# Kernel optimization log

Hardware: AMD Instinct MI355X
Metric: run time of the kernel (lower is better)

The kernel has to match this reference:

```python
import jax, jax.numpy as jnp
import numpy as np

N = 30000   # fluid particles
E = 480000  # edges
F = 4       # fluidFeatures (in channels)
P = 8       # RBF basis size per dim (dims=[8], 1D)
LAYERS = [32, 64, 64, 2]


def hat_basis(x, n):
    # 'linear' RBF: hat functions on n evenly spaced centers in [-1, 1]
    centers = jnp.linspace(-1.0, 1.0, n, dtype=x.dtype)
    spacing = 2.0 / (n - 1)
    return jnp.maximum(0.0, 1.0 - jnp.abs(x[:, None] - centers[None, :]) / spacing)  # [E, n]


def rbf_conv(x, fi, fj, d, W, b, mask, n_nodes):
    # x: [N, Cin]; d: [E, 1] clamped; W: [P, Cin, Cout]; b: [Cout]
    phi = hat_basis(d[:, 0], W.shape[0])      # [E, P]
    xj = x[fj]                                 # gather source features [E, Cin]
    msg = jnp.zeros((xj.shape[0], W.shape[2]), dtype=x.dtype)
    for p in range(W.shape[0]):                # small fixed P=8 loop keeps memory O(E*Cout)
        msg = msg + phi[:, p, None] * (xj @ W[p])
    msg = jnp.where(mask[:, None], msg, 0.0)   # centerIgnore: drop self edges fi==fj
    out = jax.ops.segment_sum(msg, fi, num_segments=n_nodes)  # scatter-reduce to targets
    return out + b


def _xavier(key, shape_in, shape_out):
    lim = float(np.sqrt(6.0 / (shape_in + shape_out)))
    return jax.random.uniform(key, (shape_in, shape_out), jnp.float32, -lim, lim)


def setup_inputs() -> dict:
    key = jax.random.key(0)
    ks = jax.random.split(key, 16)
    fluidFeatures = jax.random.normal(ks[0], (N, F), jnp.float32)
    fi = jax.random.randint(ks[1], (E,), 0, N)
    fj = jax.random.randint(ks[2], (E,), 0, N)
    distances = jax.random.normal(ks[3], (E, 1), jnp.float32)
    # conv channels: 4->32, 64->64, 64->64, 64->2
    cio = [(F, 32), (2 * 32, 64), (64, 64), (64, 2)]
    inp = {"fluidFeatures": fluidFeatures, "fi": fi, "fj": fj, "distances": distances}
    for li, (ci, co) in enumerate(cio):
        inp[f"cW{li}"] = jax.random.normal(ks[4 + li], (P, ci, co), jnp.float32) * (1.0 / np.sqrt(P * ci))
        inp[f"cb{li}"] = jnp.zeros((co,), jnp.float32)
        inp[f"fW{li}"] = _xavier(ks[8 + li], ci, co)   # stored [in, out]
        inp[f"fb{li}"] = jnp.zeros((co,), jnp.float32)
    return inp


def reference(fluidFeatures, fi, fj, distances,
              cW0, cb0, fW0, fb0, cW1, cb1, fW1, fb1,
              cW2, cb2, fW2, fb2, cW3, cb3, fW3, fb3):
    n_nodes = fluidFeatures.shape[0]
    mask = fi != fj                     # centerIgnore (mask instead of filter: jit-safe)
    d = jnp.clip(distances, -1.0, 1.0)

    conv0 = rbf_conv(fluidFeatures, fi, fj, d, cW0, cb0, mask, n_nodes)  # [N, 32]
    lin0 = fluidFeatures @ fW0 + fb0                                      # [N, 32]
    ans = jnp.concatenate([lin0, conv0], axis=1)                          # [N, 64]

    # i = 1: features[0]=32 != features[1]=64 -> no residual
    ansc = jax.nn.relu(ans)
    ans = rbf_conv(ansc, fi, fj, d, cW1, cb1, mask, n_nodes) + (ansc @ fW1 + fb1)
    # i = 2: features[1]==features[2]==64 and shapes match -> residual
    ansc = jax.nn.relu(ans)
    ans = rbf_conv(ansc, fi, fj, d, cW2, cb2, mask, n_nodes) + (ansc @ fW2 + fb2) + ans
    # i = 3: 64 -> 2, no residual
    ansc = jax.nn.relu(ans)
    ans = rbf_conv(ansc, fi, fj, d, cW3, cb3, mask, n_nodes) + (ansc @ fW3 + fb3)

    return ans  # dim == 1 (dims=[8]) -> no /128
```

## Files before the change

kernel.cpp:

```cpp
#include <hip/hip_runtime.h>


#define CAP 48

typedef __attribute__((ext_vector_type(8))) short short8;
typedef __attribute__((ext_vector_type(4))) short short4v;
typedef __attribute__((ext_vector_type(4))) float f32x4;
typedef int v4i __attribute__((ext_vector_type(4)));

__device__ __forceinline__ short bf16s(float f) {
  unsigned u = __float_as_uint(f);
  return (short)((u + 0x7FFF + ((u >> 16) & 1)) >> 16);
}
__device__ __forceinline__ float b2f(unsigned short s) {
  return __uint_as_float(((unsigned)s) << 16);
}
__device__ __forceinline__ unsigned pack2(float a, float b) {
  return (unsigned)(unsigned short)bf16s(a) | ((unsigned)(unsigned short)bf16s(b) << 16);
}
__device__ __forceinline__ float dec_w0(int v) {
  return __uint_as_float(0x3F800000u | (((unsigned)v & 0xFFFu) << 11)) - 1.0f;
}
__device__ __forceinline__ float dec_sf(int v) {
  return (float)(((unsigned)v >> 12) & 1u);
}
__device__ __forceinline__ unsigned long long rfl64(unsigned long long x) {
  unsigned lo = __builtin_amdgcn_readfirstlane((unsigned)x);
  unsigned hi = __builtin_amdgcn_readfirstlane((unsigned)(x >> 32));
  return ((unsigned long long)hi << 32) | (unsigned long long)lo;
}
__device__ __forceinline__ void gload_lds4(const void* g, void* l) {
  __builtin_amdgcn_global_load_lds(
      (const __attribute__((address_space(1))) void*)g,
      (__attribute__((address_space(3))) void*)l, 4, 0, 0);
}

#define WAIT_VM0 asm volatile("s_waitcnt vmcnt(0)" ::: "memory")
#define WAIT_LGKM0 asm volatile("s_waitcnt lgkmcnt(0)" ::: "memory")

#define LOAD_RECS32Q(JROW, CPTR, MRAW)                                      \
  v4i q0, q1, q2, q3, q4, q5, q6, q7;                                       \
  int MRAW;                                                                 \
  asm volatile("s_load_dwordx4 %0, %9, 0x0\n\t"                             \
               "s_load_dwordx4 %1, %9, 0x10\n\t"                            \
               "s_load_dwordx4 %2, %9, 0x20\n\t"                            \
               "s_load_dwordx4 %3, %9, 0x30\n\t"                            \
               "s_load_dwordx4 %4, %9, 0x40\n\t"                            \
               "s_load_dwordx4 %5, %9, 0x50\n\t"                            \
               "s_load_dwordx4 %6, %9, 0x60\n\t"                            \
               "s_load_dwordx4 %7, %9, 0x70\n\t"                            \
               "s_load_dword %8, %10, 0x0\n\t"                              \
               "s_waitcnt lgkmcnt(0)"                                       \
               : "=&s"(q0), "=&s"(q1), "=&s"(q2), "=&s"(q3), "=&s"(q4),     \
                 "=&s"(q5), "=&s"(q6), "=&s"(q7), "=&s"(MRAW)               \
               : "s"(JROW), "s"(CPTR)                                       \
               : "memory")

#define LOAD_RECS16TQ(JROW)                                                 \
  v4i qt0, qt1, qt2, qt3;                                                   \
  asm volatile("s_load_dwordx4 %0, %4, 0x80\n\t"                            \
               "s_load_dwordx4 %1, %4, 0x90\n\t"                            \
               "s_load_dwordx4 %2, %4, 0xA0\n\t"                            \
               "s_load_dwordx4 %3, %4, 0xB0\n\t"                            \
               "s_waitcnt lgkmcnt(0)"                                       \
               : "=&s"(qt0), "=&s"(qt1), "=&s"(qt2), "=&s"(qt3)             \
               : "s"(JROW)                                                  \
               : "memory")

#define RECK(K) ((K) < 4 ? q0[(K) & 3] : (K) < 8 ? q1[(K) & 3] :            \
                 (K) < 12 ? q2[(K) & 3] : (K) < 16 ? q3[(K) & 3] :          \
                 (K) < 20 ? q4[(K) & 3] : (K) < 24 ? q5[(K) & 3] :          \
                 (K) < 28 ? q6[(K) & 3] : q7[(K) & 3])
#define RECT(K) ((K) < 4 ? qt0[(K) & 3] : (K) < 8 ? qt1[(K) & 3] :          \
                 (K) < 12 ? qt2[(K) & 3] : qt3[(K) & 3])

__global__ void fill_prep(const float* __restrict__ dist,
                          const int* __restrict__ fi, const int* __restrict__ fj,
                          int* __restrict__ cnt, int* __restrict__ jw, int nE,
                          const float* __restrict__ cW1, const float* __restrict__ fW1,
                          const float* __restrict__ cW2, const float* __restrict__ fW2,
                          short* __restrict__ wt1, short* __restrict__ wt2,
                          const float* __restrict__ X,
                          const float* __restrict__ cW0,
                          const float* __restrict__ fW0,
                          unsigned short* __restrict__ U0, int n,
                          int fillBlocks, int prepBlocks) {
  if ((int)blockIdx.x < fillBlocks) {
    int e = blockIdx.x * blockDim.x + threadIdx.x;
    if (e >= nE) return;
    int i = fi[e], j = fj[e];
    if (i == j) return;
    float d = fminf(1.0f, fmaxf(-1.0f, dist[e]));
    float u = (d + 1.0f) * 3.5f;
    int p = min((int)u, 6);
    float w0 = 1.0f - (u - (float)p);
    int wq = min((int)(w0 * 4096.0f + 0.5f), 4095);
    unsigned off = (unsigned)(j * 9 + p);
    int pos = atomicAdd(&cnt[i], 1);
    if (pos < CAP)
      jw[(size_t)i * CAP + pos] = (int)((off << 13) | 0x1000u | (unsigned)wq);
  } else if ((int)blockIdx.x < fillBlocks + prepBlocks) {
    int idx = ((int)blockIdx.x - fillBlocks) * blockDim.x + threadIdx.x;
    if (idx >= 2 * 576 * 64) return;
    int sel = idx / (576 * 64);
    int r = idx - sel * (576 * 64);
    int col = r >> 6, ch = r & 63;
    const float* cW = sel ? cW2 : cW1;
    const float* fW = sel ? fW2 : fW1;
    float v;
    if (col < 512) {
      int p = col >> 6, co = col & 63;
      v = cW[((size_t)p * 64 + ch) * 64 + co];
    } else {
      v = fW[(size_t)ch * 64 + (col - 512)];
    }
    (sel ? wt2 : wt1)[(size_t)col * 64 + ch] = bf16s(v);
  } else {
    int idx = ((int)blockIdx.x - fillBlocks - prepBlocks) * blockDim.x + threadIdx.x;
    if (idx >= n * 72) return;
    int i = idx / 72, g = idx - i * 72;
    float4 x = *(const float4*)(X + (size_t)i * 4);
    float xk[4] = {x.x, x.y, x.z, x.w};
    float s[4] = {0, 0, 0, 0};
    if (g < 64) {
      int p = g >> 3;
      int co = (g * 4) & 31;
      #pragma unroll
      for (int k = 0; k < 4; ++k) {
        const float* wr = cW0 + ((size_t)p * 4 + k) * 32 + co;
        #pragma unroll
        for (int c = 0; c < 4; ++c) s[c] = fmaf(xk[k], wr[c], s[c]);
      }
    } else {
      int co = (g - 64) * 4;
      #pragma unroll
      for (int k = 0; k < 4; ++k) {
        const float* wr = fW0 + (size_t)k * 32 + co;
        #pragma unroll
        for (int c = 0; c < 4; ++c) s[c] = fmaf(xk[k], wr[c], s[c]);
      }
    }
    uint2 pk = make_uint2(pack2(s[0], s[1]), pack2(s[2], s[3]));
    *(uint2*)(U0 + (size_t)i * 288 + g * 4) = pk;
  }
}

__device__ __forceinline__ void gemm_tail8(const unsigned short* sXa, short* sUL,
                                           const short* __restrict__ WT,
                                           int w, int lane) {
  const int mrow = lane & 15;
  const int quad = lane >> 4;
  short8 b0 = *(const short8*)(sXa + mrow * 64 + quad * 8);
  short8 b1 = *(const short8*)(sXa + mrow * 64 + quad * 8 + 32);
  for (int t = w; t < 36; t += 8) {
    const short* A = WT + (size_t)(t * 16 + mrow) * 64 + quad * 8;
    short8 a0 = *(const short8*)(A);
    short8 a1 = *(const short8*)(A + 32);
    f32x4 acc = {0, 0, 0, 0};
    acc = __builtin_amdgcn_mfma_f32_16x16x32_bf16(a0, b0, acc, 0, 0, 0);
    acc = __builtin_amdgcn_mfma_f32_16x16x32_bf16(a1, b1, acc, 0, 0, 0);
    short4v pk;
    #pragma unroll
    for (int r = 0; r < 4; ++r) pk[r] = bf16s(acc[r]);
    *(short4v*)(sUL + mrow * 584 + t * 16 + quad * 4) = pk;
  }
}

__global__ __launch_bounds__(512, 8) void layer0_gemm(
    const unsigned short* __restrict__ U0,
    const int* __restrict__ cnt, const int* __restrict__ jw,
    const float* __restrict__ cb0, const float* __restrict__ fb0,
    const short* __restrict__ WTul,
    unsigned short* __restrict__ UL, int n) {
  __shared__ __align__(16) char smem[8 * 4096];
  __shared__ __align__(16) unsigned short sXa[16 * 64];
  const int tid = threadIdx.x;
  const int w = tid >> 6;
  const int lane = tid & 63;
  const int grp = lane >> 5;
  const int gl = lane & 31;
  const unsigned gl4 = (unsigned)gl * 4u;
  const int nodeBase = blockIdx.x * 8;
  const int i = nodeBase + w;
  const bool valid = (i < n);
  const int ic = valid ? i : 0;
  if (tid < 256) ((unsigned*)sXa)[256 + tid] = 0u;
  const int* jrow = (const int*)rfl64((unsigned long long)(jw + (size_t)ic * CAP));
  const int* cptr = (const int*)rfl64((unsigned long long)(cnt + ic));
  LOAD_RECS32Q(jrow, cptr, mraw);
  const int m = valid ? min(mraw, CAP) : 0;
  char* ldsW = smem + w * 4096;
  unsigned* ldsWu = (unsigned*)ldsW;
  const char* u0B = (const char*)U0;
  float accLo = 0.0f, accHi = 0.0f;
#define L0_ISSUE(K, RE)                                                     \
  { int v_ = grp ? RE(2 * (K) + 1) : RE(2 * (K));                           \
    unsigned soff_ = (((unsigned)v_) >> 7) & 0xFFFFFFC0u;                   \
    gload_lds4(u0B + soff_ + gl4, ldsW + (K) * 256); }
#define L0_CONS(K, RE)                                                      \
  { int v_ = grp ? RE(2 * (K) + 1) : RE(2 * (K));                           \
    float w0_ = dec_w0(v_);                                                 \
    float wgt_ = (gl < 16) ? w0_ : (dec_sf(v_) - w0_);                      \
    unsigned rd_ = ldsWu[(K) * 64 + lane];                                  \
    accLo = fmaf(wgt_, __uint_as_float(rd_ << 16), accLo);                  \
    accHi = fmaf(wgt_, __uint_as_float(rd_ & 0xFFFF0000u), accHi); }
  if (m > 0) {
    if (m <= 16) {
      #pragma unroll
      for (int k = 0; k < 8; ++k) L0_ISSUE(k, RECK);
      WAIT_VM0;
      #pragma unroll
      for (int k = 0; k < 8; ++k) L0_CONS(k, RECK);
    } else {
      #pragma unroll
      for (int k = 0; k < 16; ++k) L0_ISSUE(k, RECK);
      WAIT_VM0;
      #pragma unroll
      for (int k = 0; k < 16; ++k) L0_CONS(k, RECK);
      if (m > 32) {
        LOAD_RECS16TQ(jrow);
        WAIT_LGKM0;
        #pragma unroll
        for (int k = 0; k < 8; ++k) L0_ISSUE(k, RECT);
        WAIT_VM0;
        #pragma unroll
        for (int k = 0; k < 8; ++k) L0_CONS(k, RECT);
      }
    }
  }
#undef L0_ISSUE
#undef L0_CONS
  accLo += __shfl_xor(accLo, 16, 64);
  accHi += __shfl_xor(accHi, 16, 64);
  accLo += __shfl_xor(accLo, 32, 64);
  accHi += __shfl_xor(accHi, 32, 64);
  if (lane < 16) {
    const int l = lane;
    float c0v = fmaxf(accLo + cb0[2 * l], 0.0f);
    float c1v = fmaxf(accHi + cb0[2 * l + 1], 0.0f);
    unsigned lr = ((const unsigned*)(U0 + (size_t)ic * 288 + 256))[l];
    float l0 = fmaxf(__uint_as_float(lr << 16) + fb0[2 * l], 0.0f);
    float l1 = fmaxf(__uint_as_float(lr & 0xFFFF0000u) + fb0[2 * l + 1], 0.0f);
    unsigned* row = (unsigned*)(sXa + w * 64);
    row[l] = pack2(l0, l1);
    row[16 + l] = pack2(c0v, c1v);
  }
  __syncthreads();

  gemm_tail8(sXa, (short*)smem, WTul, w, lane);
  __syncthreads();
  const int r2 = tid >> 6;
  const int c0 = tid & 63;
  if (nodeBase + r2 < n) {
    const short* sUL = (const short*)smem;
    unsigned short* dst = UL + (size_t)(nodeBase + r2) * 576;
    #pragma unroll
    for (int chunk = c0; chunk < 72; chunk += 64)
      *(short8*)(dst + chunk * 8) = *(const short8*)(sUL + r2 * 584 + chunk * 8);
  }
}

__global__ __launch_bounds__(512, 8) void conv_gemm(
    const unsigned short* __restrict__ ULA,
    const int* __restrict__ cnt, const int* __restrict__ jw,
    const float* __restrict__ cb, const float* __restrict__ fb,
    const short* __restrict__ WTul2,
    float* __restrict__ outAns,
    unsigned short* __restrict__ ULB, int n) {
  __shared__ __align__(16) char smem[8 * 4096];
  __shared__ __align__(16) unsigned short sXa[16 * 64];
  const int tid = threadIdx.x;
  const int w = tid >> 6;
  const int lane = tid & 63;
  const int half = lane >> 5;
  const int pl = lane & 31;
  const unsigned lane4 = (unsigned)lane * 4u;
  const int nodeBase = blockIdx.x * 8;
  const int i = nodeBase + w;
  const bool valid = (i < n);
  const int ic = valid ? i : 0;
  if (tid < 256) ((unsigned*)sXa)[256 + tid] = 0u;
  const int* jrow = (const int*)rfl64((unsigned long long)(jw + (size_t)ic * CAP));
  const int* cptr = (const int*)rfl64((unsigned long long)(cnt + ic));
  LOAD_RECS32Q(jrow, cptr, mraw);
  const int m = valid ? min(mraw, CAP) : 0;
  const unsigned Lraw = ((const unsigned*)(ULA + (size_t)ic * 576 + 512))[pl];
  char* ldsW = smem + w * 4096;
  unsigned* ldsWu = (unsigned*)ldsW;
  const char* ulB = (const char*)ULA;
  float accLo = 0.0f, accHi = 0.0f;
#define CV_ISSUE(K, RE)                                                     \
  { unsigned soff_ = (((unsigned)RE(K)) >> 6) & 0xFFFFFF80u;                \
    gload_lds4(ulB + soff_ + lane4, ldsW + ((K) & 15) * 256); }
#define CV_CONS(K, RE)                                                      \
  { int v_ = RE(K);                                                         \
    float w0_ = dec_w0(v_);                                                 \
    float wv_ = half ? (dec_sf(v_) - w0_) : w0_;                            \
    unsigned rd_ = ldsWu[((K) & 15) * 64 + lane];                           \
    accLo = fmaf(wv_, __uint_as_float(rd_ << 16), accLo);                   \
    accHi = fmaf(wv_, __uint_as_float(rd_ & 0xFFFF0000u), accHi); }
  if (m > 0) {
    #pragma unroll
    for (int k = 0; k < 16; ++k) CV_ISSUE(k, RECK);
    WAIT_VM0;
    #pragma unroll
    for (int k = 0; k < 16; ++k) CV_CONS(k, RECK);
    if (m > 16) {
      WAIT_LGKM0;
      #pragma unroll
      for (int k = 16; k < 32; ++k) CV_ISSUE(k, RECK);
      WAIT_VM0;
      #pragma unroll
      for (int k = 16; k < 32; ++k) CV_CONS(k, RECK);
      if (m > 32) {
        LOAD_RECS16TQ(jrow);
        WAIT_LGKM0;
        #pragma unroll
        for (int k = 0; k < 16; ++k) CV_ISSUE(k, RECT);
        WAIT_VM0;
        #pragma unroll
        for (int k = 0; k < 16; ++k) CV_CONS(k, RECT);
      }
    }
  }
#undef CV_ISSUE
#undef CV_CONS
  accLo += __shfl_xor(accLo, 32, 64);
  accHi += __shfl_xor(accHi, 32, 64);
  if (half == 0) {
    unsigned* row = (unsigned*)(sXa + w * 64);
    if (valid) {
      const int c0i = 2 * pl, c1i = c0i + 1;
      float o0 = accLo + __uint_as_float(Lraw << 16) + cb[c0i] + fb[c0i];
      float o1 = accHi + __uint_as_float(Lraw & 0xFFFF0000u) + cb[c1i] + fb[c1i];
      *(float2*)(outAns + (size_t)i * 64 + c0i) = make_float2(o0, o1);
      row[pl] = pack2(fmaxf(o0, 0.0f), fmaxf(o1, 0.0f));
    } else {
      row[pl] = 0u;
    }
  }
  __syncthreads();

  gemm_tail8(sXa, (short*)smem, WTul2, w, lane);
  __syncthreads();
  const int r2 = tid >> 6;
  const int c0 = tid & 63;
  if (nodeBase + r2 < n) {
    const short* sUL = (const short*)smem;
    unsigned short* dst = ULB + (size_t)(nodeBase + r2) * 576;
    #pragma unroll
    for (int chunk = c0; chunk < 72; chunk += 64)
      *(short8*)(dst + chunk * 8) = *(const short8*)(sUL + r2 * 584 + chunk * 8);
  }
}

__global__ __launch_bounds__(256, 8) void conv2_kernel(
    const unsigned short* __restrict__ UL,
    const int* __restrict__ cnt, const int* __restrict__ jw,
    const float* __restrict__ cb, const float* __restrict__ fb,
    const float* __restrict__ resid,
    const float* __restrict__ cW3,
    float* __restrict__ T,
    unsigned short* __restrict__ outAnsc, int n) {
  __shared__ __align__(16) char smem2[4 * 4096];
  const int lane = threadIdx.x & 63;
  const int half = lane >> 5;
  const int pl = lane & 31;
  const unsigned lane4 = (unsigned)lane * 4u;
  const int w4 = threadIdx.x >> 6;
  const int i = (blockIdx.x * blockDim.x + threadIdx.x) >> 6;
  if (i >= n) return;
  const int* jrow = (const int*)rfl64((unsigned long long)(jw + (size_t)i * CAP));
  const int* cptr = (const int*)rfl64((unsigned long long)(cnt + i));
  LOAD_RECS32Q(jrow, cptr, mraw);
  const int m = min(mraw, CAP);
  const unsigned Lraw = ((const unsigned*)(UL + (size_t)i * 576 + 512))[pl];
  float2 rv = *(const float2*)(resid + (size_t)i * 64 + 2 * pl);
  char* ldsW = smem2 + w4 * 4096;
  unsigned* ldsWu = (unsigned*)ldsW;
  const char* ulB = (const char*)UL;
  float accLo = 0.0f, accHi = 0.0f;
#define CV_ISSUE(K, RE)                                                     \
  { unsigned soff_ = (((unsigned)RE(K)) >> 6) & 0xFFFFFF80u;                \
    gload_lds4(ulB + soff_ + lane4, ldsW + ((K) & 15) * 256); }
#define CV_CONS(K, RE)                                                      \
  { int v_ = RE(K);                                                         \
    float w0_ = dec_w0(v_);                                                 \
    float wv_ = half ? (dec_sf(v_) - w0_) : w0_;                            \
    unsigned rd_ = ldsWu[((K) & 15) * 64 + lane];                           \
    accLo = fmaf(wv_, __uint_as_float(rd_ << 16), accLo);                   \
    accHi = fmaf(wv_, __uint_as_float(rd_ & 0xFFFF0000u), accHi); }
  if (m > 0) {
    #pragma unroll
    for (int k = 0; k < 16; ++k) CV_ISSUE(k, RECK);
    WAIT_VM0;
    #pragma unroll
    for (int k = 0; k < 16; ++k) CV_CONS(k, RECK);
    if (m > 16) {
      WAIT_LGKM0;
      #pragma unroll
      for (int k = 16; k < 32; ++k) CV_ISSUE(k, RECK);
      WAIT_VM0;
      #pragma unroll
      for (int k = 16; k < 32; ++k) CV_CONS(k, RECK);
      if (m > 32) {
        LOAD_RECS16TQ(jrow);
        WAIT_LGKM0;
        #pragma unroll
        for (int k = 0; k < 16; ++k) CV_ISSUE(k, RECT);
        WAIT_VM0;
        #pragma unroll
        for (int k = 0; k < 16; ++k) CV_CONS(k, RECT);
      }
    }
  }
#undef CV_ISSUE
#undef CV_CONS
  accLo += __shfl_xor(accLo, 32, 64);
  accHi += __shfl_xor(accHi, 32, 64);
  if (half == 0) {
    const int c0i = 2 * pl, c1i = c0i + 1;
    float o0 = accLo + __uint_as_float(Lraw << 16) + cb[c0i] + fb[c0i] + rv.x;
    float o1 = accHi + __uint_as_float(Lraw & 0xFFFF0000u) + cb[c1i] + fb[c1i] + rv.y;
    unsigned short xb0 = (unsigned short)bf16s(fmaxf(o0, 0.0f));
    unsigned short xb1 = (unsigned short)bf16s(fmaxf(o1, 0.0f));
    ((unsigned*)(outAnsc + (size_t)i * 64))[pl] = (unsigned)xb0 | ((unsigned)xb1 << 16);
    float x0 = b2f(xb0), x1 = b2f(xb1);
    float c[16];
    #pragma unroll
    for (int t = 0; t < 16; ++t) {
      const float* wrow = cW3 + ((size_t)(t >> 1) * 64) * 2 + (t & 1);
      c[t] = x0 * wrow[c0i * 2] + x1 * wrow[c1i * 2];
    }
    #pragma unroll
    for (int off = 16; off > 0; off >>= 1) {
      #pragma unroll
      for (int t = 0; t < 16; ++t) c[t] += __shfl_xor(c[t], off, 64);
    }
    if (pl == 0) {
      float* tr = T + (size_t)i * 18;
      #pragma unroll
      for (int t = 0; t < 16; ++t) tr[t] = c[t];
    }
  }
}

__global__ __launch_bounds__(256, 4) void layer3_kernel(
    const unsigned short* __restrict__ Xb,
    const float* __restrict__ T,
    const int* __restrict__ cnt, const int* __restrict__ jw,
    const float* __restrict__ cb3, const float* __restrict__ fb3,
    const float* __restrict__ fW3,
    float* __restrict__ out, int n) {
  const int lane = threadIdx.x & 63;
  const int i = (blockIdx.x * blockDim.x + threadIdx.x) >> 6;
  if (i >= n) return;
  const int m = min(cnt[i], CAP);
  float c0 = 0.0f, c1 = 0.0f;
  if (lane < m) {
    int v = jw[(size_t)i * CAP + lane];
    unsigned off = (unsigned)v >> 13;
    float w0 = dec_w0(v);
    float w1 = 1.0f - w0;
    const float* tb = T + (size_t)off * 2;
    float2 ta = *(const float2*)(tb);
    float2 tc = *(const float2*)(tb + 2);
    c0 = w0 * ta.x + w1 * tc.x;
    c1 = w0 * ta.y + w1 * tc.y;
  }
  float xi = b2f(Xb[(size_t)i * 64 + lane]);
  float2 fw = *(const float2*)(fW3 + lane * 2);
  c0 = fmaf(xi, fw.x, c0);
  c1 = fmaf(xi, fw.y, c1);
  #pragma unroll
  for (int off = 32; off > 0; off >>= 1) {
    c0 += __shfl_xor(c0, off, 64);
    c1 += __shfl_xor(c1, off, 64);
  }
  if (lane == 0) {
    out[(size_t)i * 2 + 0] = c0 + cb3[0] + fb3[0];
    out[(size_t)i * 2 + 1] = c1 + cb3[1] + fb3[1];
  }
}

extern "C" void kernel_launch(void* const* d_in, const int* in_sizes, int n_in,
                              void* d_out, int out_size, void* d_ws, size_t ws_size,
                              hipStream_t stream) {
  const float* X    = (const float*)d_in[0];
  const int*   fi   = (const int*)d_in[1];
  const int*   fj   = (const int*)d_in[2];
  const float* dist = (const float*)d_in[3];
  const float* cW0 = (const float*)d_in[4];  const float* cb0 = (const float*)d_in[5];
  const float* fW0 = (const float*)d_in[6];  const float* fb0 = (const float*)d_in[7];
  const float* cW1 = (const float*)d_in[8];  const float* cb1 = (const float*)d_in[9];
  const float* fW1 = (const float*)d_in[10]; const float* fb1 = (const float*)d_in[11];
  const float* cW2 = (const float*)d_in[12]; const float* cb2 = (const float*)d_in[13];
  const float* fW2 = (const float*)d_in[14]; const float* fb2 = (const float*)d_in[15];
  const float* cW3 = (const float*)d_in[16]; const float* cb3 = (const float*)d_in[17];
  const float* fW3 = (const float*)d_in[18]; const float* fb3 = (const float*)d_in[19];
  float* out = (float*)d_out;

  const int n  = in_sizes[0] / 4;
  const int nE = in_sizes[1];

  unsigned short* ULA   = (unsigned short*)d_ws;
  unsigned short* ULB   = ULA + (size_t)n * 576;
  unsigned short* U0    = ULB;
  float*          ans1  = (float*)(ULB + (size_t)n * 576);
  unsigned short* ansc2 = (unsigned short*)(ans1 + (size_t)n * 64);
  float* T     = (float*)(ansc2 + (size_t)n * 64);
  short* wtul1 = (short*)(T + (size_t)n * 18);
  short* wtul2 = wtul1 + 576 * 64;
  int*   jw    = (int*)(wtul2 + 576 * 64);
  int*   cnt   = jw + (size_t)n * CAP;

  hipMemsetAsync(jw, 0, ((size_t)n * CAP + n) * sizeof(int), stream);
  const int fillBlocks = (nE + 255) / 256;
  const int prepBlocks = (2 * 576 * 64 + 255) / 256;
  const int u0Blocks   = (n * 72 + 255) / 256;
  fill_prep<<<fillBlocks + prepBlocks + u0Blocks, 256, 0, stream>>>(
      dist, fi, fj, cnt, jw, nE, cW1, fW1, cW2, fW2, wtul1, wtul2,
      X, cW0, fW0, U0, n, fillBlocks, prepBlocks);

  layer0_gemm<<<(n + 7) / 8, 512, 0, stream>>>(U0, cnt, jw, cb0, fb0,
                                               wtul1, ULA, n);
  conv_gemm<<<(n + 7) / 8, 512, 0, stream>>>(ULA, cnt, jw, cb1, fb1,
                                             wtul2, ans1, ULB, n);
  conv2_kernel<<<(n * 64 + 255) / 256, 256, 0, stream>>>(
      ULB, cnt, jw, cb2, fb2, ans1, cW3, T, ansc2, n);
  layer3_kernel<<<(n * 64 + 255) / 256, 256, 0, stream>>>(ansc2, T, cnt, jw,
                                                          cb3, fb3, fW3, out, n);
}
```

Before: 268.0 us.

## Aggregate raw features per basis bin before GEMM instead of transforming-then-gathering

Swaps the order of the conv math. The old version transformed each node's features into a 576-wide per-basis bf16 table and then gathered that wide table per edge. The new version gathers the 64-channel source features per edge, accumulates them into 8 hat-basis bins, and then runs one 576-deep MFMA GEMM per 16-node tile. This cuts per-edge gather traffic from 576 to 64 bf16 values, drops the large intermediate UL arrays, and fuses the layer-3 cW3 projection into the layer-2 kernel via MFMA. In exchange, every edge now does 64-lane gathers with a switch-based bin accumulation, blocks use 1024 threads, and the GEMM does more work per node.

```diff
diff --git a/kernel.cpp b/kernel.cpp
--- a/kernel.cpp
+++ b/kernel.cpp
@@ -4,7 +4,6 @@
 #define CAP 48
 
 typedef __attribute__((ext_vector_type(8))) short short8;
-typedef __attribute__((ext_vector_type(4))) short short4v;
 typedef __attribute__((ext_vector_type(4))) float f32x4;
 typedef int v4i __attribute__((ext_vector_type(4)));
 
@@ -29,14 +28,6 @@
   unsigned hi = __builtin_amdgcn_readfirstlane((unsigned)(x >> 32));
   return ((unsigned long long)hi << 32) | (unsigned long long)lo;
 }
-__device__ __forceinline__ void gload_lds4(const void* g, void* l) {
-  __builtin_amdgcn_global_load_lds(
-      (const __attribute__((address_space(1))) void*)g,
-      (__attribute__((address_space(3))) void*)l, 4, 0, 0);
-}
-
-#define WAIT_VM0 asm volatile("s_waitcnt vmcnt(0)" ::: "memory")
-#define WAIT_LGKM0 asm volatile("s_waitcnt lgkmcnt(0)" ::: "memory")
 
 #define LOAD_RECS32Q(JROW, CPTR, MRAW)                                      \
   v4i q0, q1, q2, q3, q4, q5, q6, q7;                                       \
@@ -77,13 +68,14 @@
 __global__ void fill_prep(const float* __restrict__ dist,
                           const int* __restrict__ fi, const int* __restrict__ fj,
                           int* __restrict__ cnt, int* __restrict__ jw, int nE,
+                          const float* __restrict__ cW0, const float* __restrict__ fW0,
                           const float* __restrict__ cW1, const float* __restrict__ fW1,
                           const float* __restrict__ cW2, const float* __restrict__ fW2,
-                          short* __restrict__ wt1, short* __restrict__ wt2,
+                          const float* __restrict__ cW3,
+                          short* __restrict__ W0T, short* __restrict__ W1T,
+                          short* __restrict__ W2T, short* __restrict__ WT3,
                           const float* __restrict__ X,
-                          const float* __restrict__ cW0,
-                          const float* __restrict__ fW0,
-                          unsigned short* __restrict__ U0, int n,
+                          unsigned short* __restrict__ Xb, int n,
                           int fillBlocks, int prepBlocks) {
   if ((int)blockIdx.x < fillBlocks) {
     int e = blockIdx.x * blockDim.x + threadIdx.x;
@@ -95,352 +87,250 @@
     int p = min((int)u, 6);
     float w0 = 1.0f - (u - (float)p);
     int wq = min((int)(w0 * 4096.0f + 0.5f), 4095);
-    unsigned off = (unsigned)(j * 9 + p);
     int pos = atomicAdd(&cnt[i], 1);
     if (pos < CAP)
-      jw[(size_t)i * CAP + pos] = (int)((off << 13) | 0x1000u | (unsigned)wq);
+      jw[(size_t)i * CAP + pos] =
+          (int)(((unsigned)j << 17) | ((unsigned)p << 14) | 0x1000u | (unsigned)wq);
   } else if ((int)blockIdx.x < fillBlocks + prepBlocks) {
     int idx = ((int)blockIdx.x - fillBlocks) * blockDim.x + threadIdx.x;
-    if (idx >= 2 * 576 * 64) return;
-    int sel = idx / (576 * 64);
-    int r = idx - sel * (576 * 64);
-    int col = r >> 6, ch = r & 63;
-    const float* cW = sel ? cW2 : cW1;
-    const float* fW = sel ? fW2 : fW1;
-    float v;
-    if (col < 512) {
-      int p = col >> 6, co = col & 63;
-      v = cW[((size_t)p * 64 + ch) * 64 + co];
-    } else {
-      v = fW[(size_t)ch * 64 + (col - 512)];
-    }
-    (sel ? wt2 : wt1)[(size_t)col * 64 + ch] = bf16s(v);
+    if (idx < 36864) {
+      int o = idx / 576, k = idx - o * 576;
+      float v = (k < 512) ? cW1[((size_t)(k >> 6) * 64 + (k & 63)) * 64 + o]
+                          : fW1[(size_t)(k - 512) * 64 + o];
+      W1T[idx] = bf16s(v);
+    } else if (idx < 73728) {
+      int r = idx - 36864;
+      int o = r / 576, k = r - o * 576;
+      float v = (k < 512) ? cW2[((size_t)(k >> 6) * 64 + (k & 63)) * 64 + o]
+                          : fW2[(size_t)(k - 512) * 64 + o];
+      W2T[r] = bf16s(v);
+    } else if (idx < 77824) {
+      int r = idx - 73728;
+      int o = r >> 6, k = r & 63;
+      float v = 0.0f;
+      if (o < 32) {
+        if (k >= 60) v = fW0[(size_t)(k - 60) * 32 + o];
+      } else {
+        if ((k & 7) < 4 && k < 60)
+          v = cW0[((size_t)(k >> 3) * 4 + (k & 7)) * 32 + (o - 32)];
+      }
+      W0T[r] = bf16s(v);
+    } else if (idx < 78848) {
+      int r = idx - 77824;
+      int t = r >> 6, ch = r & 63;
+      WT3[r] = bf16s(cW3[((size_t)(t >> 1) * 64 + ch) * 2 + (t & 1)]);
+    }
   } else {
     int idx = ((int)blockIdx.x - fillBlocks - prepBlocks) * blockDim.x + threadIdx.x;
-    if (idx >= n * 72) return;
-    int i = idx / 72, g = idx - i * 72;
-    float4 x = *(const float4*)(X + (size_t)i * 4);
-    float xk[4] = {x.x, x.y, x.z, x.w};
-    float s[4] = {0, 0, 0, 0};
-    if (g < 64) {
-      int p = g >> 3;
-      int co = (g * 4) & 31;
-      #pragma unroll
-      for (int k = 0; k < 4; ++k) {
-        const float* wr = cW0 + ((size_t)p * 4 + k) * 32 + co;
-        #pragma unroll
-        for (int c = 0; c < 4; ++c) s[c] = fmaf(xk[k], wr[c], s[c]);
-      }
-    } else {
-      int co = (g - 64) * 4;
-      #pragma unroll
-      for (int k = 0; k < 4; ++k) {
-        const float* wr = fW0 + (size_t)k * 32 + co;
-        #pragma unroll
-        for (int c = 0; c < 4; ++c) s[c] = fmaf(xk[k], wr[c], s[c]);
-      }
-    }
-    uint2 pk = make_uint2(pack2(s[0], s[1]), pack2(s[2], s[3]));
-    *(uint2*)(U0 + (size_t)i * 288 + g * 4) = pk;
-  }
-}
-
-__device__ __forceinline__ void gemm_tail8(const unsigned short* sXa, short* sUL,
-                                           const short* __restrict__ WT,
-                                           int w, int lane) {
-  const int mrow = lane & 15;
-  const int quad = lane >> 4;
-  short8 b0 = *(const short8*)(sXa + mrow * 64 + quad * 8);
-  short8 b1 = *(const short8*)(sXa + mrow * 64 + quad * 8 + 32);
-  for (int t = w; t < 36; t += 8) {
-    const short* A = WT + (size_t)(t * 16 + mrow) * 64 + quad * 8;
-    short8 a0 = *(const short8*)(A);
-    short8 a1 = *(const short8*)(A + 32);
-    f32x4 acc = {0, 0, 0, 0};
-    acc = __builtin_amdgcn_mfma_f32_16x16x32_bf16(a0, b0, acc, 0, 0, 0);
-    acc = __builtin_amdgcn_mfma_f32_16x16x32_bf16(a1, b1, acc, 0, 0, 0);
-    short4v pk;
-    #pragma unroll
-    for (int r = 0; r < 4; ++r) pk[r] = bf16s(acc[r]);
-    *(short4v*)(sUL + mrow * 584 + t * 16 + quad * 4) = pk;
-  }
-}
-
-__global__ __launch_bounds__(512, 8) void layer0_gemm(
-    const unsigned short* __restrict__ U0,
+    if (idx >= n * 8) return;
+    int i = idx >> 3, c = idx & 7;
+    float v = (c < 4) ? X[(size_t)i * 4 + c] : 0.0f;
+    Xb[idx] = (unsigned short)bf16s(v);
+  }
+}
+
+__global__ __launch_bounds__(1024, 8) void layer0_gemm(
+    const unsigned short* __restrict__ Xb,
     const int* __restrict__ cnt, const int* __restrict__ jw,
     const float* __restrict__ cb0, const float* __restrict__ fb0,
-    const short* __restrict__ WTul,
-    unsigned short* __restrict__ UL, int n) {
-  __shared__ __align__(16) char smem[8 * 4096];
-  __shared__ __align__(16) unsigned short sXa[16 * 64];
+    const short* __restrict__ W0T,
+    unsigned short* __restrict__ ansc0, int n) {
+  __shared__ __align__(16) unsigned short sA0[16 * 72];
   const int tid = threadIdx.x;
   const int w = tid >> 6;
   const int lane = tid & 63;
-  const int grp = lane >> 5;
-  const int gl = lane & 31;
-  const unsigned gl4 = (unsigned)gl * 4u;
-  const int nodeBase = blockIdx.x * 8;
+  const int s_lane = lane >> 3;
+  const int k_lane = lane & 7;
+  const int nodeBase = blockIdx.x * 16;
   const int i = nodeBase + w;
   const bool valid = (i < n);
   const int ic = valid ? i : 0;
-  if (tid < 256) ((unsigned*)sXa)[256 + tid] = 0u;
   const int* jrow = (const int*)rfl64((unsigned long long)(jw + (size_t)ic * CAP));
   const int* cptr = (const int*)rfl64((unsigned long long)(cnt + ic));
   LOAD_RECS32Q(jrow, cptr, mraw);
   const int m = valid ? min(mraw, CAP) : 0;
-  char* ldsW = smem + w * 4096;
-  unsigned* ldsWu = (unsigned*)ldsW;
-  const char* u0B = (const char*)U0;
-  float accLo = 0.0f, accHi = 0.0f;
-#define L0_ISSUE(K, RE)                                                     \
-  { int v_ = grp ? RE(2 * (K) + 1) : RE(2 * (K));                           \
-    unsigned soff_ = (((unsigned)v_) >> 7) & 0xFFFFFFC0u;                   \
-    gload_lds4(u0B + soff_ + gl4, ldsW + (K) * 256); }
-#define L0_CONS(K, RE)                                                      \
-  { int v_ = grp ? RE(2 * (K) + 1) : RE(2 * (K));                           \
+  float acc = 0.0f;
+#define L0E(K, RE)                                                          \
+  { int v_ = RE(K);                                                         \
+    const unsigned short* rp_ = Xb + ((size_t)((unsigned)v_ >> 17) << 3);   \
+    float xv_ = b2f(rp_[k_lane]);                                           \
     float w0_ = dec_w0(v_);                                                 \
-    float wgt_ = (gl < 16) ? w0_ : (dec_sf(v_) - w0_);                      \
-    unsigned rd_ = ldsWu[(K) * 64 + lane];                                  \
-    accLo = fmaf(wgt_, __uint_as_float(rd_ << 16), accLo);                  \
-    accHi = fmaf(wgt_, __uint_as_float(rd_ & 0xFFFF0000u), accHi); }
-  if (m > 0) {
-    if (m <= 16) {
+    float w1_ = dec_sf(v_) - w0_;                                           \
+    int p_ = (int)(((unsigned)v_ >> 14) & 7u);                              \
+    float sel_ = (s_lane == p_) ? w0_ : ((s_lane == p_ + 1) ? w1_ : 0.0f);  \
+    acc = fmaf(sel_, xv_, acc); }
+  L0E(0, RECK) L0E(1, RECK) L0E(2, RECK) L0E(3, RECK)
+  L0E(4, RECK) L0E(5, RECK) L0E(6, RECK) L0E(7, RECK)
+  L0E(8, RECK) L0E(9, RECK) L0E(10, RECK) L0E(11, RECK)
+  L0E(12, RECK) L0E(13, RECK) L0E(14, RECK) L0E(15, RECK)
+  if (m > 16) {
+    L0E(16, RECK) L0E(17, RECK) L0E(18, RECK) L0E(19, RECK)
+    L0E(20, RECK) L0E(21, RECK) L0E(22, RECK) L0E(23, RECK)
+    L0E(24, RECK) L0E(25, RECK) L0E(26, RECK) L0E(27, RECK)
+    L0E(28, RECK) L0E(29, RECK) L0E(30, RECK) L0E(31, RECK)
+    if (m > 32) {
+      LOAD_RECS16TQ(jrow);
+      L0E(0, RECT) L0E(1, RECT) L0E(2, RECT) L0E(3, RECT)
+      L0E(4, RECT) L0E(5, RECT) L0E(6, RECT) L0E(7, RECT)
+      L0E(8, RECT) L0E(9, RECT) L0E(10, RECT) L0E(11, RECT)
+      L0E(12, RECT) L0E(13, RECT) L0E(14, RECT) L0E(15, RECT)
+    }
+  }
+#undef L0E
+  float aout = acc;
+  if (lane >= 60) aout = b2f(Xb[(size_t)ic * 8 + (lane - 60)]);
+  sA0[w * 72 + lane] = (unsigned short)bf16s(aout);
+  __syncthreads();
+  if (w < 4) {
+    const int mrow = lane & 15, quad = lane >> 4, t = w;
+    short8 b0 = *(const short8*)(sA0 + mrow * 72 + quad * 8);
+    short8 b1 = *(const short8*)(sA0 + mrow * 72 + quad * 8 + 32);
+    short8 a0 = *(const short8*)(W0T + (size_t)(t * 16 + mrow) * 64 + quad * 8);
+    short8 a1 = *(const short8*)(W0T + (size_t)(t * 16 + mrow) * 64 + quad * 8 + 32);
+    f32x4 acc4 = {0, 0, 0, 0};
+    acc4 = __builtin_amdgcn_mfma_f32_16x16x32_bf16(a0, b0, acc4, 0, 0, 0);
+    acc4 = __builtin_amdgcn_mfma_f32_16x16x32_bf16(a1, b1, acc4, 0, 0, 0);
+    const int node2 = nodeBase + mrow;
+    const int ch0 = t * 16 + quad * 4;
+    if (node2 < n) {
+      float vv[4];
       #pragma unroll
-      for (int k = 0; k < 8; ++k) L0_ISSUE(k, RECK);
-      WAIT_VM0;
-      #pragma unroll
-      for (int k = 0; k < 8; ++k) L0_CONS(k, RECK);
-    } else {
-      #pragma unroll
-      for (int k = 0; k < 16; ++k) L0_ISSUE(k, RECK);
-      WAIT_VM0;
-      #pragma unroll
-      for (int k = 0; k < 16; ++k) L0_CONS(k, RECK);
-      if (m > 32) {
-        LOAD_RECS16TQ(jrow);
-        WAIT_LGKM0;
-        #pragma unroll
-        for (int k = 0; k < 8; ++k) L0_ISSUE(k, RECT);
-        WAIT_VM0;
-        #pragma unroll
-        for (int k = 0; k < 8; ++k) L0_CONS(k, RECT);
+      for (int r = 0; r < 4; ++r) {
+        int ch = ch0 + r;
+        float bias = (ch < 32) ? fb0[ch] : cb0[ch - 32];
+        vv[r] = fmaxf(acc4[r] + bias, 0.0f);
       }
-    }
-  }
-#undef L0_ISSUE
-#undef L0_CONS
-  accLo += __shfl_xor(accLo, 16, 64);
-  accHi += __shfl_xor(accHi, 16, 64);
-  accLo += __shfl_xor(accLo, 32, 64);
-  accHi += __shfl_xor(accHi, 32, 64);
-  if (lane < 16) {
-    const int l = lane;
-    float c0v = fmaxf(accLo + cb0[2 * l], 0.0f);
-    float c1v = fmaxf(accHi + cb0[2 * l + 1], 0.0f);
-    unsigned lr = ((const unsigned*)(U0 + (size_t)ic * 288 + 256))[l];
-    float l0 = fmaxf(__uint_as_float(lr << 16) + fb0[2 * l], 0.0f);
-    float l1 = fmaxf(__uint_as_float(lr & 0xFFFF0000u) + fb0[2 * l + 1], 0.0f);
-    unsigned* row = (unsigned*)(sXa + w * 64);
-    row[l] = pack2(l0, l1);
-    row[16 + l] = pack2(c0v, c1v);
-  }
-  __syncthreads();
-
-  gemm_tail8(sXa, (short*)smem, WTul, w, lane);
-  __syncthreads();
-  const int r2 = tid >> 6;
-  const int c0 = tid & 63;
-  if (nodeBase + r2 < n) {
-    const short* sUL = (const short*)smem;
-    unsigned short* dst = UL + (size_t)(nodeBase + r2) * 576;
-    #pragma unroll
-    for (int chunk = c0; chunk < 72; chunk += 64)
-      *(short8*)(dst + chunk * 8) = *(const short8*)(sUL + r2 * 584 + chunk * 8);
-  }
-}
-
-__global__ __launch_bounds__(512, 8) void conv_gemm(
-    const unsigned short* __restrict__ ULA,
+      *(uint2*)(ansc0 + (size_t)node2 * 64 + ch0) =
+          make_uint2(pack2(vv[0], vv[1]), pack2(vv[2], vv[3]));
+    }
+  }
+}
+
+__global__ __launch_bounds__(1024, 8) void conv_agg(
+    const unsigned short* __restrict__ ancPrev,
     const int* __restrict__ cnt, const int* __restrict__ jw,
+    const short* __restrict__ WTn,
     const float* __restrict__ cb, const float* __restrict__ fb,
-    const short* __restrict__ WTul2,
-    float* __restrict__ outAns,
-    unsigned short* __restrict__ ULB, int n) {
-  __shared__ __align__(16) char smem[8 * 4096];
-  __shared__ __align__(16) unsigned short sXa[16 * 64];
+    const float* __restrict__ resid,
+    float* __restrict__ outF32,
+    unsigned short* __restrict__ outAnsc,
+    const short* __restrict__ WT3,
+    float* __restrict__ T, int flags, int n) {
+  __shared__ __align__(16) unsigned short sA[16 * 584];
+  __shared__ __align__(16) unsigned short sC[16 * 72];
   const int tid = threadIdx.x;
   const int w = tid >> 6;
   const int lane = tid & 63;
-  const int half = lane >> 5;
-  const int pl = lane & 31;
-  const unsigned lane4 = (unsigned)lane * 4u;
-  const int nodeBase = blockIdx.x * 8;
+  const int nodeBase = blockIdx.x * 16;
   const int i = nodeBase + w;
   const bool valid = (i < n);
   const int ic = valid ? i : 0;
-  if (tid < 256) ((unsigned*)sXa)[256 + tid] = 0u;
   const int* jrow = (const int*)rfl64((unsigned long long)(jw + (size_t)ic * CAP));
   const int* cptr = (const int*)rfl64((unsigned long long)(cnt + ic));
   LOAD_RECS32Q(jrow, cptr, mraw);
   const int m = valid ? min(mraw, CAP) : 0;
-  const unsigned Lraw = ((const unsigned*)(ULA + (size_t)ic * 576 + 512))[pl];
-  char* ldsW = smem + w * 4096;
-  unsigned* ldsWu = (unsigned*)ldsW;
-  const char* ulB = (const char*)ULA;
-  float accLo = 0.0f, accHi = 0.0f;
-#define CV_ISSUE(K, RE)                                                     \
-  { unsigned soff_ = (((unsigned)RE(K)) >> 6) & 0xFFFFFF80u;                \
-    gload_lds4(ulB + soff_ + lane4, ldsW + ((K) & 15) * 256); }
-#define CV_CONS(K, RE)                                                      \
+  const unsigned short own = ancPrev[(size_t)ic * 64 + lane];
+  float a0 = 0, a1 = 0, a2 = 0, a3 = 0, a4 = 0, a5 = 0, a6 = 0, a7 = 0;
+#define CVE(K, RE)                                                          \
   { int v_ = RE(K);                                                         \
+    const unsigned short* rp_ = ancPrev + ((size_t)((unsigned)v_ >> 17) << 6); \
+    float xv_ = b2f(rp_[lane]);                                             \
     float w0_ = dec_w0(v_);                                                 \
-    float wv_ = half ? (dec_sf(v_) - w0_) : w0_;                            \
-    unsigned rd_ = ldsWu[((K) & 15) * 64 + lane];                           \
-    accLo = fmaf(wv_, __uint_as_float(rd_ << 16), accLo);                   \
-    accHi = fmaf(wv_, __uint_as_float(rd_ & 0xFFFF0000u), accHi); }
-  if (m > 0) {
+    float w1_ = dec_sf(v_) - w0_;                                           \
+    switch (((unsigned)v_ >> 14) & 7u) {                                    \
+      case 0: a0 = fmaf(w0_, xv_, a0); a1 = fmaf(w1_, xv_, a1); break;      \
+      case 1: a1 = fmaf(w0_, xv_, a1); a2 = fmaf(w1_, xv_, a2); break;      \
+      case 2: a2 = fmaf(w0_, xv_, a2); a3 = fmaf(w1_, xv_, a3); break;      \
+      case 3: a3 = fmaf(w0_, xv_, a3); a4 = fmaf(w1_, xv_, a4); break;      \
+      case 4: a4 = fmaf(w0_, xv_, a4); a5 = fmaf(w1_, xv_, a5); break;      \
+      case 5: a5 = fmaf(w0_, xv_, a5); a6 = fmaf(w1_, xv_, a6); break;      \
+      case 6: a6 = fmaf(w0_, xv_, a6); a7 = fmaf(w1_, xv_, a7); break;      \
+      default: break;                                                       \
+    } }
+  CVE(0, RECK) CVE(1, RECK) CVE(2, RECK) CVE(3, RECK)
+  CVE(4, RECK) CVE(5, RECK) CVE(6, RECK) CVE(7, RECK)
+  CVE(8, RECK) CVE(9, RECK) CVE(10, RECK) CVE(11, RECK)
+  CVE(12, RECK) CVE(13, RECK) CVE(14, RECK) CVE(15, RECK)
+  if (m > 16) {
+    CVE(16, RECK) CVE(17, RECK) CVE(18, RECK) CVE(19, RECK)
+    CVE(20, RECK) CVE(21, RECK) CVE(22, RECK) CVE(23, RECK)
+    CVE(24, RECK) CVE(25, RECK) CVE(26, RECK) CVE(27, RECK)
+    CVE(28, RECK) CVE(29, RECK) CVE(30, RECK) CVE(31, RECK)
+    if (m > 32) {
+      LOAD_RECS16TQ(jrow);
+      CVE(0, RECT) CVE(1, RECT) CVE(2, RECT) CVE(3, RECT)
+      CVE(4, RECT) CVE(5, RECT) CVE(6, RECT) CVE(7, RECT)
+      CVE(8, RECT) CVE(9, RECT) CVE(10, RECT) CVE(11, RECT)
+      CVE(12, RECT) CVE(13, RECT) CVE(14, RECT) CVE(15, RECT)
+    }
+  }
+#undef CVE
+  {
+    unsigned short* sAr = sA + w * 584;
+    sAr[0 * 64 + lane] = (unsigned short)bf16s(a0);
+    sAr[1 * 64 + lane] = (unsigned short)bf16s(a1);
+    sAr[2 * 64 + lane] = (unsigned short)bf16s(a2);
+    sAr[3 * 64 + lane] = (unsigned short)bf16s(a3);
+    sAr[4 * 64 + lane] = (unsigned short)bf16s(a4);
+    sAr[5 * 64 + lane] = (unsigned short)bf16s(a5);
+    sAr[6 * 64 + lane] = (unsigned short)bf16s(a6);
+    sAr[7 * 64 + lane] = (unsigned short)bf16s(a7);
+    sAr[512 + lane] = own;
+  }
+  __syncthreads();
+  if (w < 4) {
+    const int mrow = lane & 15, quad = lane >> 4, t = w;
+    f32x4 acc4 = {0, 0, 0, 0};
+    const short* arow = WTn + (size_t)(t * 16 + mrow) * 576 + quad * 8;
+    const unsigned short* brow = sA + mrow * 584 + quad * 8;
     #pragma unroll
-    for (int k = 0; k < 16; ++k) CV_ISSUE(k, RECK);
-    WAIT_VM0;
-    #pragma unroll
-    for (int k = 0; k < 16; ++k) CV_CONS(k, RECK);
-    if (m > 16) {
-      WAIT_LGKM0;
-      #pragma unroll
-      for (int k = 16; k < 32; ++k) CV_ISSUE(k, RECK);
-      WAIT_VM0;
-      #pragma unroll
-      for (int k = 16; k < 32; ++k) CV_CONS(k, RECK);
-      if (m > 32) {
-        LOAD_RECS16TQ(jrow);
-        WAIT_LGKM0;
-        #pragma unroll
-        for (int k = 0; k < 16; ++k) CV_ISSUE(k, RECT);
-        WAIT_VM0;
-        #pragma unroll
-        for (int k = 0; k < 16; ++k) CV_CONS(k, RECT);
+    for (int kk = 0; kk < 18; ++kk) {
+      short8 af = *(const short8*)(arow + kk * 32);
+      short8 bf = *(const short8*)(brow + kk * 32);
+      acc4 = __builtin_amdgcn_mfma_f32_16x16x32_bf16(af, bf, acc4, 0, 0, 0);
+    }
+    const int node2 = nodeBase + mrow;
+    const int ch0 = t * 16 + quad * 4;
+    if (node2 < n) {
+      float4 rv = make_float4(0.f, 0.f, 0.f, 0.f);
+      if (flags & 1) rv = *(const float4*)(resid + (size_t)node2 * 64 + ch0);
+      float v0 = acc4[0] + cb[ch0 + 0] + fb[ch0 + 0] + rv.x;
+      float v1 = acc4[1] + cb[ch0 + 1] + fb[ch0 + 1] + rv.y;
+      float v2 = acc4[2] + cb[ch0 + 2] + fb[ch0 + 2] + rv.z;
+      float v3 = acc4[3] + cb[ch0 + 3] + fb[ch0 + 3] + rv.w;
+      if (flags & 2) {
+        *(float2*)(outF32 + (size_t)node2 * 64 + ch0) = make_float2(v0, v1);
+        *(float2*)(outF32 + (size_t)node2 * 64 + ch0 + 2) = make_float2(v2, v3);
       }
-    }
-  }
-#undef CV_ISSUE
-#undef CV_CONS
-  accLo += __shfl_xor(accLo, 32, 64);
-  accHi += __shfl_xor(accHi, 32, 64);
-  if (half == 0) {
-    unsigned* row = (unsigned*)(sXa + w * 64);
-    if (valid) {
-      const int c0i = 2 * pl, c1i = c0i + 1;
-      float o0 = accLo + __uint_as_float(Lraw << 16) + cb[c0i] + fb[c0i];
-      float o1 = accHi + __uint_as_float(Lraw & 0xFFFF0000u) + cb[c1i] + fb[c1i];
-      *(float2*)(outAns + (size_t)i * 64 + c0i) = make_float2(o0, o1);
-      row[pl] = pack2(fmaxf(o0, 0.0f), fmaxf(o1, 0.0f));
-    } else {
-      row[pl] = 0u;
-    }
-  }
-  __syncthreads();
-
-  gemm_tail8(sXa, (short*)smem, WTul2, w, lane);
-  __syncthreads();
-  const int r2 = tid >> 6;
-  const int c0 = tid & 63;
-  if (nodeBase + r2 < n) {
-    const short* sUL = (const short*)smem;
-    unsigned short* dst = ULB + (size_t)(nodeBase + r2) * 576;
-    #pragma unroll
-    for (int chunk = c0; chunk < 72; chunk += 64)
-      *(short8*)(dst + chunk * 8) = *(const short8*)(sUL + r2 * 584 + chunk * 8);
-  }
-}
-
-__global__ __launch_bounds__(256, 8) void conv2_kernel(
-    const unsigned short* __restrict__ UL,
-    const int* __restrict__ cnt, const int* __restrict__ jw,
-    const float* __restrict__ cb, const float* __restrict__ fb,
-    const float* __restrict__ resid,
-    const float* __restrict__ cW3,
-    float* __restrict__ T,
-    unsigned short* __restrict__ outAnsc, int n) {
-  __shared__ __align__(16) char smem2[4 * 4096];
-  const int lane = threadIdx.x & 63;
-  const int half = lane >> 5;
-  const int pl = lane & 31;
-  const unsigned lane4 = (unsigned)lane * 4u;
-  const int w4 = threadIdx.x >> 6;
-  const int i = (blockIdx.x * blockDim.x + threadIdx.x) >> 6;
-  if (i >= n) return;
-  const int* jrow = (const int*)rfl64((unsigned long long)(jw + (size_t)i * CAP));
-  const int* cptr = (const int*)rfl64((unsigned long long)(cnt + i));
-  LOAD_RECS32Q(jrow, cptr, mraw);
-  const int m = min(mraw, CAP);
-  const unsigned Lraw = ((const unsigned*)(UL + (size_t)i * 576 + 512))[pl];
-  float2 rv = *(const float2*)(resid + (size_t)i * 64 + 2 * pl);
-  char* ldsW = smem2 + w4 * 4096;
-  unsigned* ldsWu = (unsigned*)ldsW;
-  const char* ulB = (const char*)UL;
-  float accLo = 0.0f, accHi = 0.0f;
-#define CV_ISSUE(K, RE)                                                     \
-  { unsigned soff_ = (((unsigned)RE(K)) >> 6) & 0xFFFFFF80u;                \
-    gload_lds4(ulB + soff_ + lane4, ldsW + ((K) & 15) * 256); }
-#define CV_CONS(K, RE)                                                      \
-  { int v_ = RE(K);                                                         \
-    float w0_ = dec_w0(v_);                                                 \
-    float wv_ = half ? (dec_sf(v_) - w0_) : w0_;                            \
-    unsigned rd_ = ldsWu[((K) & 15) * 64 + lane];                           \
-    accLo = fmaf(wv_, __uint_as_float(rd_ << 16), accLo);                   \
-    accHi = fmaf(wv_, __uint_as_float(rd_ & 0xFFFF0000u), accHi); }
-  if (m > 0) {
-    #pragma unroll
-    for (int k = 0; k < 16; ++k) CV_ISSUE(k, RECK);
-    WAIT_VM0;
-    #pragma unroll
-    for (int k = 0; k < 16; ++k) CV_CONS(k, RECK);
-    if (m > 16) {
-      WAIT_LGKM0;
-      #pragma unroll
-      for (int k = 16; k < 32; ++k) CV_ISSUE(k, RECK);
-      WAIT_VM0;
-      #pragma unroll
-      for (int k = 16; k < 32; ++k) CV_CONS(k, RECK);
-      if (m > 32) {
-        LOAD_RECS16TQ(jrow);
-        WAIT_LGKM0;
-        #pragma unroll
-        for (int k = 0; k < 16; ++k) CV_ISSUE(k, RECT);
-        WAIT_VM0;
-        #pragma unroll
-        for (int k = 0; k < 16; ++k) CV_CONS(k, RECT);
+      unsigned lo = pack2(fmaxf(v0, 0.f), fmaxf(v1, 0.f));
+      unsigned hi = pack2(fmaxf(v2, 0.f), fmaxf(v3, 0.f));
+      *(uint2*)(outAnsc + (size_t)node2 * 64 + ch0) = make_uint2(lo, hi);
+      if (flags & 4) {
+        *(unsigned*)(sC + mrow * 72 + ch0) = lo;
+        *(unsigned*)(sC + mrow * 72 + ch0 + 2) = hi;
       }
-    }
-  }
-#undef CV_ISSUE
-#undef CV_CONS
-  accLo += __shfl_xor(accLo, 32, 64);
-  accHi += __shfl_xor(accHi, 32, 64);
-  if (half == 0) {
-    const int c0i = 2 * pl, c1i = c0i + 1;
-    float o0 = accLo + __uint_as_float(Lraw << 16) + cb[c0i] + fb[c0i] + rv.x;
-    float o1 = accHi + __uint_as_float(Lraw & 0xFFFF0000u) + cb[c1i] + fb[c1i] + rv.y;
-    unsigned short xb0 = (unsigned short)bf16s(fmaxf(o0, 0.0f));
-    unsigned short xb1 = (unsigned short)bf16s(fmaxf(o1, 0.0f));
-    ((unsigned*)(outAnsc + (size_t)i * 64))[pl] = (unsigned)xb0 | ((unsigned)xb1 << 16);
-    float x0 = b2f(xb0), x1 = b2f(xb1);
-    float c[16];
-    #pragma unroll
-    for (int t = 0; t < 16; ++t) {
-      const float* wrow = cW3 + ((size_t)(t >> 1) * 64) * 2 + (t & 1);
-      c[t] = x0 * wrow[c0i * 2] + x1 * wrow[c1i * 2];
-    }
-    #pragma unroll
-    for (int off = 16; off > 0; off >>= 1) {
-      #pragma unroll
-      for (int t = 0; t < 16; ++t) c[t] += __shfl_xor(c[t], off, 64);
-    }
-    if (pl == 0) {
-      float* tr = T + (size_t)i * 18;
-      #pragma unroll
-      for (int t = 0; t < 16; ++t) tr[t] = c[t];
+    } else if (flags & 4) {
+      *(unsigned*)(sC + mrow * 72 + ch0) = 0u;
+      *(unsigned*)(sC + mrow * 72 + ch0 + 2) = 0u;
+    }
+  }
+  if (flags & 4) {
+    __syncthreads();
+    if (w == 0) {
+      const int mrow = lane & 15, quad = lane >> 4;
+      short8 b0 = *(const short8*)(sC + mrow * 72 + quad * 8);
+      short8 b1 = *(const short8*)(sC + mrow * 72 + quad * 8 + 32);
+      short8 a0v = *(const short8*)(WT3 + mrow * 64 + quad * 8);
+      short8 a1v = *(const short8*)(WT3 + mrow * 64 + quad * 8 + 32);
+      f32x4 acc4 = {0, 0, 0, 0};
+      acc4 = __builtin_amdgcn_mfma_f32_16x16x32_bf16(a0v, b0, acc4, 0, 0, 0);
+      acc4 = __builtin_amdgcn_mfma_f32_16x16x32_bf16(a1v, b1, acc4, 0, 0, 0);
+      const int node2 = nodeBase + mrow;
+      if (node2 < n) {
+        float* tr = T + (size_t)node2 * 18 + quad * 4;
+        *(float2*)(tr) = make_float2(acc4[0], acc4[1]);
+        *(float2*)(tr + 2) = make_float2(acc4[2], acc4[3]);
+      }
     }
   }
 }
@@ -459,10 +349,12 @@
   float c0 = 0.0f, c1 = 0.0f;
   if (lane < m) {
     int v = jw[(size_t)i * CAP + lane];
-    unsigned off = (unsigned)v >> 13;
+    unsigned j = (unsigned)v >> 17;
+    unsigned p = ((unsigned)v >> 14) & 7u;
+    unsigned off9 = j * 9u + p;
     float w0 = dec_w0(v);
     float w1 = 1.0f - w0;
-    const float* tb = T + (size_t)off * 2;
+    const float* tb = T + (size_t)off9 * 2;
     float2 ta = *(const float2*)(tb);
     float2 tc = *(const float2*)(tb + 2);
     c0 = w0 * ta.x + w1 * tc.x;
@@ -503,31 +395,36 @@
   const int n  = in_sizes[0] / 4;
   const int nE = in_sizes[1];
 
-  unsigned short* ULA   = (unsigned short*)d_ws;
-  unsigned short* ULB   = ULA + (size_t)n * 576;
-  unsigned short* U0    = ULB;
-  float*          ans1  = (float*)(ULB + (size_t)n * 576);
-  unsigned short* ansc2 = (unsigned short*)(ans1 + (size_t)n * 64);
-  float* T     = (float*)(ansc2 + (size_t)n * 64);
-  short* wtul1 = (short*)(T + (size_t)n * 18);
-  short* wtul2 = wtul1 + 576 * 64;
-  int*   jw    = (int*)(wtul2 + 576 * 64);
-  int*   cnt   = jw + (size_t)n * CAP;
+  unsigned short* ansc0 = (unsigned short*)d_ws;
+  float*          ans1  = (float*)(ansc0 + (size_t)n * 64);
+  unsigned short* ansc1 = (unsigned short*)(ans1 + (size_t)n * 64);
+  unsigned short* ansc2 = ansc1 + (size_t)n * 64;
+  float*          T     = (float*)(ansc2 + (size_t)n * 64);
+  unsigned short* Xb16  = (unsigned short*)(T + (size_t)n * 18);
+  short* W1T = (short*)(Xb16 + (size_t)n * 8);
+  short* W2T = W1T + 36864;
+  short* W0T = W2T + 36864;
+  short* WT3 = W0T + 4096;
+  int*   jw  = (int*)(WT3 + 1024);
+  int*   cnt = jw + (size_t)n * CAP;
 
   hipMemsetAsync(jw, 0, ((size_t)n * CAP + n) * sizeof(int), stream);
   const int fillBlocks = (nE + 255) / 256;
-  const int prepBlocks = (2 * 576 * 64 + 255) / 256;
-  const int u0Blocks   = (n * 72 + 255) / 256;
-  fill_prep<<<fillBlocks + prepBlocks + u0Blocks, 256, 0, stream>>>(
-      dist, fi, fj, cnt, jw, nE, cW1, fW1, cW2, fW2, wtul1, wtul2,
-      X, cW0, fW0, U0, n, fillBlocks, prepBlocks);
-
-  layer0_gemm<<<(n + 7) / 8, 512, 0, stream>>>(U0, cnt, jw, cb0, fb0,
-                                               wtul1, ULA, n);
-  conv_gemm<<<(n + 7) / 8, 512, 0, stream>>>(ULA, cnt, jw, cb1, fb1,
-                                             wtul2, ans1, ULB, n);
-  conv2_kernel<<<(n * 64 + 255) / 256, 256, 0, stream>>>(
-      ULB, cnt, jw, cb2, fb2, ans1, cW3, T, ansc2, n);
+  const int prepBlocks = (78848 + 255) / 256;
+  const int xbBlocks   = (n * 8 + 255) / 256;
+  fill_prep<<<fillBlocks + prepBlocks + xbBlocks, 256, 0, stream>>>(
+      dist, fi, fj, cnt, jw, nE, cW0, fW0, cW1, fW1, cW2, fW2, cW3,
+      W0T, W1T, W2T, WT3, X, Xb16, n, fillBlocks, prepBlocks);
+
+  const int nodeBlocks = (n + 15) / 16;
+  layer0_gemm<<<nodeBlocks, 1024, 0, stream>>>(Xb16, cnt, jw, cb0, fb0,
+                                               W0T, ansc0, n);
+  conv_agg<<<nodeBlocks, 1024, 0, stream>>>(ansc0, cnt, jw, W1T, cb1, fb1,
+                                            ans1 , ans1, ansc1,
+                                            WT3, T, 2, n);
+  conv_agg<<<nodeBlocks, 1024, 0, stream>>>(ansc1, cnt, jw, W2T, cb2, fb2,
+                                            ans1, ans1, ansc2,
+                                            WT3, T, 5, n);
   layer3_kernel<<<(n * 64 + 255) / 256, 256, 0, stream>>>(ansc2, T, cnt, jw,
                                                           cb3, fb3, fW3, out, n);
 }
```

After: 268.9 us. No clear change (+0.3%).
